# Optimization experiments

Measured on AMD Instinct MI355X. Metric: run time of the kernel, lower is better.

Reference implementation:

```python
import jax, jax.numpy as jnp
import numpy as np

B, S, C, V, LAT, NL = 256, 512, 256, 32, 256, 7
DILS = [1, 2, 4, 8, 16, 32, 64]
EPS = 1e-5


def setup_inputs() -> dict:
    key = jax.random.key(0)
    ks = jax.random.split(key, 24)
    s = 0.05
    inp = {
        "x": jax.random.randint(ks[0], (B, S), 0, V, dtype=jnp.int64 if jax.config.read("jax_enable_x64") else jnp.int32),
        "z": jax.random.normal(ks[1], (B, LAT), dtype=jnp.float32),
        "emb": jax.random.normal(ks[2], (V, C), dtype=jnp.float32) * s,
        "latent_W": jax.random.normal(ks[3], (LAT, C), dtype=jnp.float32) * s,
        "latent_b": jnp.zeros((C,), jnp.float32),
        "ln1_g": jnp.ones((NL, C), jnp.float32),
        "ln1_b": jnp.zeros((NL, C), jnp.float32),
        "w1": jax.random.normal(ks[4], (NL, C, C), jnp.float32) * s,
        "b1": jnp.zeros((NL, C), jnp.float32),
        "ln2_g": jnp.ones((NL, C), jnp.float32),
        "ln2_b": jnp.zeros((NL, C), jnp.float32),
        "wd": jax.random.normal(ks[5], (NL, 2, C, C), jnp.float32) * s,  # tap 0 = x[t-d], tap 1 = x[t]
        "bd": jnp.zeros((NL, C), jnp.float32),
        "ln3_g": jnp.ones((NL, C), jnp.float32),
        "ln3_b": jnp.zeros((NL, C), jnp.float32),
        "we": jax.random.normal(ks[6], (NL, C, C), jnp.float32) * s,
        "be": jnp.zeros((NL, C), jnp.float32),
        "wg": jax.random.normal(ks[7], (NL, C, C), jnp.float32) * s,
        "bg": jnp.zeros((NL, C), jnp.float32),
        "out_W": jax.random.normal(ks[8], (C, V), jnp.float32) * s,
        "out_b": jnp.zeros((V,), jnp.float32),
    }
    return inp


def _ln(h, g, b):
    mu = h.mean(-1, keepdims=True)
    var = jnp.mean((h - mu) ** 2, axis=-1, keepdims=True)
    return (h - mu) * jax.lax.rsqrt(var + EPS) * g + b


def _lrelu(h):
    return jnp.where(h >= 0, h, 0.01 * h)


def reference(x, z, emb, latent_W, latent_b, ln1_g, ln1_b, w1, b1,
              ln2_g, ln2_b, wd, bd, ln3_g, ln3_b, we, be, wg, bg,
              out_W, out_b):
    # channel-last layout [B, S, C] throughout (fuses away the torch transposes)
    h = emb[x] + (z @ latent_W + latent_b)[:, None, :]
    for i, d in enumerate(DILS):
        x_inp = h
        t = _lrelu(_ln(x_inp, ln1_g[i], ln1_b[i]))
        t = t @ w1[i] + b1[i]
        t = _lrelu(_ln(t, ln2_g[i], ln2_b[i]))
        # causal dilated conv, kernel=2: out[t] = W0*x[t-d] + W1*x[t]
        t_shift = jnp.pad(t, ((0, 0), (d, 0), (0, 0)))[:, :t.shape[1], :]
        t = t_shift @ wd[i, 0] + t @ wd[i, 1] + bd[i]
        t = _lrelu(_ln(t, ln3_g[i], ln3_b[i]))
        gated = (t @ we[i] + be[i]) * jax.nn.sigmoid(t @ wg[i] + bg[i])
        h = gated + x_inp
    logits = h @ out_W + out_b                      # [B, S, V]
    lp = jax.nn.log_softmax(logits, axis=-1)
    # gather log-prob of next token: lp[:, :-1, :] at x[:, 1:]
    return jnp.take_along_axis(lp[:, :-1, :], x[:, 1:, None], axis=2)[..., 0]
```

## Files before the change

### kernel.cpp

```cpp
#include <hip/hip_runtime.h>

typedef unsigned short u16;
typedef unsigned int   u32;
typedef __attribute__((ext_vector_type(8))) short short8;
typedef __attribute__((ext_vector_type(4))) float f32x4;

struct __align__(8) u16x4 { u16 x, y, z, w; };

#define NL 7
#define M_DIM 131072

__device__ __forceinline__ float b2f(u16 u) {
  union { float f; u32 i; } c; c.i = ((u32)u) << 16; return c.f;
}
__device__ __forceinline__ u16 f2b(float f) {
  union { float f; u32 i; } c; c.f = f;
  u32 r = c.i + 0x7FFFu + ((c.i >> 16) & 1u);
  return (u16)(r >> 16);
}
__device__ __forceinline__ float wave_sum(float v) {
  #pragma unroll
  for (int off = 1; off < 64; off <<= 1) v += __shfl_xor(v, off);
  return v;
}
__device__ __forceinline__ void gload16(const void* g, void* l) {
  __builtin_amdgcn_global_load_lds((const __attribute__((address_space(1))) void*)g,
                                   (__attribute__((address_space(3))) void*)l, 16, 0, 0);
}


__global__ __launch_bounds__(256) void conv_w1_k(const float* __restrict__ w1, u16* __restrict__ wT) {
  int idx = blockIdx.x * 256 + threadIdx.x;
  int i = idx >> 16, rem = idx & 65535;
  int n = rem >> 8, k = rem & 255;
  wT[idx] = f2b(w1[(i << 16) + (k << 8) + n]);
}

__global__ __launch_bounds__(256) void conv_wd_k(const float* __restrict__ wd, u16* __restrict__ wT) {
  int idx = blockIdx.x * 256 + threadIdx.x;
  int i = idx / 131072, rem = idx & 131071;
  int n = rem >> 9, k2 = rem & 511;
  int tap = k2 >> 8, k = k2 & 255;
  wT[idx] = f2b(wd[(((i * 2 + tap) << 8) + k) * 256 + n]);
}

__global__ __launch_bounds__(256) void conv_weg_k(const float* __restrict__ we, const float* __restrict__ wg,
                                                  u16* __restrict__ wT) {
  int idx = blockIdx.x * 256 + threadIdx.x;
  int i = idx / 131072, rem = idx & 131071;
  int src = rem >> 16, n = (rem >> 8) & 255, k = rem & 255;
  const float* W = src ? wg : we;
  wT[idx] = f2b(W[((i << 8) + k) * 256 + n]);
}

__global__ __launch_bounds__(256) void conv_wo_k(const float* __restrict__ outW, u16* __restrict__ wTo) {
  int idx = blockIdx.x * 256 + threadIdx.x;
  int v = idx >> 8, k = idx & 255;
  wTo[idx] = f2b(outW[k * 32 + v]);
}


__global__ __launch_bounds__(256) void zlat_k(const float* __restrict__ z, const float* __restrict__ W,
                                              const float* __restrict__ bias, float* __restrict__ zlat) {
  int b = blockIdx.x, c = threadIdx.x;
  float acc = bias[c];
  for (int l = 0; l < 256; ++l) acc += z[b * 256 + l] * W[l * 256 + c];
  zlat[b * 256 + c] = acc;
}


__device__ __forceinline__ void ln_lrelu4(float v0, float v1, float v2, float v3,
                                          const float* __restrict__ g, const float* __restrict__ b,
                                          int c, u16x4* out) {
  float s = wave_sum(v0 + v1 + v2 + v3);
  float q = wave_sum(v0 * v0 + v1 * v1 + v2 * v2 + v3 * v3);
  float mu = s * 0.00390625f;
  float var = q * 0.00390625f - mu * mu;
  float rs = rsqrtf(var + 1e-5f);
  float4 gv = *(const float4*)&g[c];
  float4 bv = *(const float4*)&b[c];
  float y0 = (v0 - mu) * rs * gv.x + bv.x; y0 = y0 >= 0.f ? y0 : 0.01f * y0;
  float y1 = (v1 - mu) * rs * gv.y + bv.y; y1 = y1 >= 0.f ? y1 : 0.01f * y1;
  float y2 = (v2 - mu) * rs * gv.z + bv.z; y2 = y2 >= 0.f ? y2 : 0.01f * y2;
  float y3 = (v3 - mu) * rs * gv.w + bv.w; y3 = y3 >= 0.f ? y3 : 0.01f * y3;
  out->x = f2b(y0); out->y = f2b(y1); out->z = f2b(y2); out->w = f2b(y3);
}


__global__ __launch_bounds__(256) void embed_ln_k(const int* __restrict__ x, const float* __restrict__ emb,
                                                  const float* __restrict__ zlat,
                                                  const float* __restrict__ g, const float* __restrict__ b,
                                                  u16* __restrict__ h, u16* __restrict__ tOut) {
  int wave = threadIdx.x >> 6, lane = threadIdx.x & 63;
  int r = blockIdx.x * 4 + wave;
  int c = lane * 4;
  int tok = x[r];
  int bi = r >> 9;
  float4 ev = *(const float4*)&emb[tok * 256 + c];
  float4 zv = *(const float4*)&zlat[bi * 256 + c];
  float v0 = ev.x + zv.x, v1 = ev.y + zv.y, v2 = ev.z + zv.z, v3 = ev.w + zv.w;
  u16x4 hb; hb.x = f2b(v0); hb.y = f2b(v1); hb.z = f2b(v2); hb.w = f2b(v3);
  *(u16x4*)&h[(long)r * 256 + c] = hb;
  u16x4 ov;
  ln_lrelu4(v0, v1, v2, v3, g, b, c, &ov);
  *(u16x4*)&tOut[(long)r * 256 + c] = ov;
}


__global__ __launch_bounds__(512, 4) void gemm_ln_k(
    const u16* __restrict__ A, const u16* __restrict__ WT, int Ktot, int dil,
    const float* __restrict__ bias, const float* __restrict__ g, const float* __restrict__ b,
    u16* __restrict__ Out)
{
  __shared__ u16 lA[128 * 32];
  __shared__ u16 lB[256 * 32];
  __shared__ float pS[128][4], pQ[128][4];
  __shared__ float muA[128], rsA[128];
  const int tid = threadIdx.x;
  const int lane = tid & 63;
  const int wv = tid >> 6;
  const int mw = wv >> 2;
  const int nw = wv & 3;
  const int m0 = blockIdx.x * 128;
  const int rA = tid >> 2;
  const int cSw = ((((tid & 3) - ((tid >> 3) & 3)) & 3)) * 8;
  const int mm = m0 + rA;
  const int s1 = mm & 511;
  const bool fixBlk = (dil > 0) && ((m0 & 511) == 0);
  const int lr = lane & 15;
  const int quad = lane >> 4;
  const int sw = ((quad + ((lr >> 1) & 3)) & 3) * 8;

  f32x4 acc[4][4];
  #pragma unroll
  for (int i = 0; i < 4; ++i)
    #pragma unroll
    for (int j = 0; j < 4; ++j) {
      acc[i][j][0] = 0.f; acc[i][j][1] = 0.f; acc[i][j][2] = 0.f; acc[i][j][3] = 0.f;
    }

  const int nkt = Ktot >> 5;
  for (int kt = 0; kt < nkt; ++kt) {
    const int kk = (kt & 7) * 32;
    int r = mm;
    if (dil > 0 && kt < 8) r = (s1 >= dil) ? (mm - dil) : mm;
    gload16(A + (long)r * 256 + kk + cSw, &lA[tid * 8]);
    const u16* bSrc = WT + kt * 32 + cSw;
    gload16(bSrc + (long)rA * Ktot,         &lB[tid * 8]);
    gload16(bSrc + (long)(rA + 128) * Ktot, &lB[tid * 8 + 4096]);
    __syncthreads();

    if (fixBlk && kt < 8) {
      if (rA < dil) {
        uint4 zz; zz.x = 0; zz.y = 0; zz.z = 0; zz.w = 0;
        *(uint4*)&lA[rA * 32 + (tid & 3) * 8] = zz;
      }
      __syncthreads();
    }

    short8 af[4], bfr[4];
    #pragma unroll
    for (int mt = 0; mt < 4; ++mt)
      af[mt] = *(const short8*)&lA[(mw * 64 + mt * 16 + lr) * 32 + sw];
    #pragma unroll
    for (int nt = 0; nt < 4; ++nt)
      bfr[nt] = *(const short8*)&lB[(nw * 64 + nt * 16 + lr) * 32 + sw];
    #pragma unroll
    for (int mt = 0; mt < 4; ++mt)
      #pragma unroll
      for (int nt = 0; nt < 4; ++nt)
        acc[mt][nt] = __builtin_amdgcn_mfma_f32_16x16x32_bf16(af[mt], bfr[nt], acc[mt][nt], 0, 0, 0);
    __syncthreads();
  }

  float biasv[4], gv[4], bv[4];
  #pragma unroll
  for (int nt = 0; nt < 4; ++nt) {
    int n = nw * 64 + nt * 16 + lr;
    biasv[nt] = bias[n]; gv[nt] = g[n]; bv[nt] = b[n];
  }
  #pragma unroll
  for (int mt = 0; mt < 4; ++mt)
    #pragma unroll
    for (int r = 0; r < 4; ++r) {
      float s = 0.f, q = 0.f;
      #pragma unroll
      for (int nt = 0; nt < 4; ++nt) {
        float v = acc[mt][nt][r] + biasv[nt];
        acc[mt][nt][r] = v;
        s += v; q += v * v;
      }
      #pragma unroll
      for (int off = 1; off < 16; off <<= 1) {
        s += __shfl_xor(s, off); q += __shfl_xor(q, off);
      }
      if (lr == 0) {
        int row = mw * 64 + mt * 16 + quad * 4 + r;
        pS[row][nw] = s; pQ[row][nw] = q;
      }
    }
  __syncthreads();
  if (tid < 128) {
    float S = pS[tid][0] + pS[tid][1] + pS[tid][2] + pS[tid][3];
    float Q = pQ[tid][0] + pQ[tid][1] + pQ[tid][2] + pQ[tid][3];
    float mu = S * 0.00390625f;
    float var = Q * 0.00390625f - mu * mu;
    muA[tid] = mu; rsA[tid] = rsqrtf(var + 1e-5f);
  }
  __syncthreads();
  #pragma unroll
  for (int mt = 0; mt < 4; ++mt)
    #pragma unroll
    for (int r = 0; r < 4; ++r) {
      int row = mw * 64 + mt * 16 + quad * 4 + r;
      float mu = muA[row], rs = rsA[row];
      #pragma unroll
      for (int nt = 0; nt < 4; ++nt) {
        float y = (acc[mt][nt][r] - mu) * rs * gv[nt] + bv[nt];
        y = y >= 0.f ? y : 0.01f * y;
        Out[(long)(m0 + row) * 256 + nw * 64 + nt * 16 + lr] = f2b(y);
      }
    }
}


__global__ __launch_bounds__(512, 4) void gemm_gate_ln_k(
    const u16* __restrict__ P, const u16* __restrict__ WTeg,
    const float* __restrict__ be, const float* __restrict__ bg,
    const float* __restrict__ g, const float* __restrict__ b,
    u16* __restrict__ h, u16* __restrict__ tOut, int doLN)
{
  __shared__ __align__(16) char smem[39424];
  u16* lA = (u16*)smem;
  u16* lB = (u16*)(smem + 4096);
  u16* xch = (u16*)smem;
  float* pS  = (float*)(smem + 36864);
  float* pQ  = (float*)(smem + 36864 + 1024);
  float* muA = (float*)(smem + 36864 + 2048);
  float* rsA = (float*)(smem + 36864 + 2304);
  const int tid = threadIdx.x;
  const int lane = tid & 63;
  const int wv = tid >> 6;
  const int eg = wv >> 2;
  const int nw = wv & 3;
  const int m0 = blockIdx.x * 64;
  const int rA = tid >> 2;
  const int cSw = ((((tid & 3) - ((tid >> 3) & 3)) & 3)) * 8;
  const int lr = lane & 15;
  const int quad = lane >> 4;
  const int sw = ((quad + ((lr >> 1) & 3)) & 3) * 8;

  f32x4 acc[4][4];
  #pragma unroll
  for (int i = 0; i < 4; ++i)
    #pragma unroll
    for (int j = 0; j < 4; ++j) {
      acc[i][j][0] = 0.f; acc[i][j][1] = 0.f; acc[i][j][2] = 0.f; acc[i][j][3] = 0.f;
    }

  for (int kt = 0; kt < 8; ++kt) {
    const int kk = kt * 32;
    if (tid < 256)
      gload16(P + (long)(m0 + rA) * 256 + kk + cSw, &lA[tid * 8]);
    const u16* bSrc = WTeg + kk + cSw;
    #pragma unroll
    for (int j = 0; j < 4; ++j)
      gload16(bSrc + (long)(rA + j * 128) * 256, &lB[tid * 8 + j * 4096]);
    __syncthreads();

    short8 af[4], bf[4];
    #pragma unroll
    for (int mt = 0; mt < 4; ++mt)
      af[mt] = *(const short8*)&lA[(mt * 16 + lr) * 32 + sw];
    #pragma unroll
    for (int nt = 0; nt < 4; ++nt)
      bf[nt] = *(const short8*)&lB[(eg * 256 + nw * 64 + nt * 16 + lr) * 32 + sw];
    #pragma unroll
    for (int mt = 0; mt < 4; ++mt)
      #pragma unroll
      for (int nt = 0; nt < 4; ++nt)
        acc[mt][nt] = __builtin_amdgcn_mfma_f32_16x16x32_bf16(af[mt], bf[nt], acc[mt][nt], 0, 0, 0);
    __syncthreads();
  }

  float bxv[4];
  #pragma unroll
  for (int nt = 0; nt < 4; ++nt) {
    int n = nw * 64 + nt * 16 + lr;
    bxv[nt] = eg ? bg[n] : be[n];
  }
  if (eg) {
    #pragma unroll
    for (int mt = 0; mt < 4; ++mt)
      #pragma unroll
      for (int r = 0; r < 4; ++r) {
        int row = mt * 16 + quad * 4 + r;
        #pragma unroll
        for (int nt = 0; nt < 4; ++nt) {
          int n = nw * 64 + nt * 16 + lr;
          float gg = acc[mt][nt][r] + bxv[nt];
          xch[row * 264 + n] = f2b(1.f / (1.f + expf(-gg)));
        }
      }
  }
  __syncthreads();
  if (!eg) {
    #pragma unroll
    for (int mt = 0; mt < 4; ++mt)
      #pragma unroll
      for (int r = 0; r < 4; ++r) {
        int row = mt * 16 + quad * 4 + r;
        long off = (long)(m0 + row) * 256;
        float s = 0.f, q = 0.f;
        #pragma unroll
        for (int nt = 0; nt < 4; ++nt) {
          int n = nw * 64 + nt * 16 + lr;
          float e = acc[mt][nt][r] + bxv[nt];
          float sg = b2f(xch[row * 264 + n]);
          float hn = e * sg + b2f(h[off + n]);
          h[off + n] = f2b(hn);
          acc[mt][nt][r] = hn;
          s += hn; q += hn * hn;
        }
        #pragma unroll
        for (int o = 1; o < 16; o <<= 1) {
          s += __shfl_xor(s, o); q += __shfl_xor(q, o);
        }
        if (lr == 0) { pS[row * 4 + nw] = s; pQ[row * 4 + nw] = q; }
      }
  }
  __syncthreads();
  if (tid < 64) {
    float S = pS[tid * 4] + pS[tid * 4 + 1] + pS[tid * 4 + 2] + pS[tid * 4 + 3];
    float Q = pQ[tid * 4] + pQ[tid * 4 + 1] + pQ[tid * 4 + 2] + pQ[tid * 4 + 3];
    float mu = S * 0.00390625f;
    float var = Q * 0.00390625f - mu * mu;
    muA[tid] = mu; rsA[tid] = rsqrtf(var + 1e-5f);
  }
  __syncthreads();
  if (doLN && !eg) {
    float gv[4], bv[4];
    #pragma unroll
    for (int nt = 0; nt < 4; ++nt) {
      int n = nw * 64 + nt * 16 + lr;
      gv[nt] = g[n]; bv[nt] = b[n];
    }
    #pragma unroll
    for (int mt = 0; mt < 4; ++mt)
      #pragma unroll
      for (int r = 0; r < 4; ++r) {
        int row = mt * 16 + quad * 4 + r;
        float mu = muA[row], rs = rsA[row];
        #pragma unroll
        for (int nt = 0; nt < 4; ++nt) {
          float y = (acc[mt][nt][r] - mu) * rs * gv[nt] + bv[nt];
          y = y >= 0.f ? y : 0.01f * y;
          tOut[(long)(m0 + row) * 256 + nw * 64 + nt * 16 + lr] = f2b(y);
        }
      }
  }
}


__global__ __launch_bounds__(256) void final_k(const u16* __restrict__ h, const u16* __restrict__ WTo,
                                               const float* __restrict__ outb, const int* __restrict__ x,
                                               float* __restrict__ out) {
  __shared__ u16 lW[32 * 264];
  const int tid = threadIdx.x;
  const int lane = tid & 63;
  const int wv = tid >> 6;
  const int mBase = blockIdx.x * 256 + wv * 64;

  #pragma unroll
  for (int j = 0; j < 4; ++j) {
    int chunk = tid + 256 * j;
    int v = chunk >> 5, k8 = chunk & 31;
    uint4 w4 = *(const uint4*)(WTo + v * 256 + k8 * 8);
    *(uint4*)&lW[v * 264 + k8 * 8] = w4;
  }
  __syncthreads();

  const int lq = (lane >> 4) * 8;
  const int lr = lane & 15;
  const int quad = lane >> 4;

  f32x4 acc[4][2];
  #pragma unroll
  for (int mt = 0; mt < 4; ++mt) {
    acc[mt][0][0] = 0.f; acc[mt][0][1] = 0.f; acc[mt][0][2] = 0.f; acc[mt][0][3] = 0.f;
    acc[mt][1][0] = 0.f; acc[mt][1][1] = 0.f; acc[mt][1][2] = 0.f; acc[mt][1][3] = 0.f;
  }

  for (int kt = 0; kt < 8; ++kt) {
    short8 bf0 = *(const short8*)&lW[lr * 264 + kt * 32 + lq];
    short8 bf1 = *(const short8*)&lW[(16 + lr) * 264 + kt * 32 + lq];
    #pragma unroll
    for (int mt = 0; mt < 4; ++mt) {
      short8 af = *(const short8*)(h + (long)(mBase + mt * 16 + lr) * 256 + kt * 32 + lq);
      acc[mt][0] = __builtin_amdgcn_mfma_f32_16x16x32_bf16(af, bf0, acc[mt][0], 0, 0, 0);
      acc[mt][1] = __builtin_amdgcn_mfma_f32_16x16x32_bf16(af, bf1, acc[mt][1], 0, 0, 0);
    }
  }

  float ob0 = outb[lr], ob1 = outb[16 + lr];
  #pragma unroll
  for (int mt = 0; mt < 4; ++mt)
    #pragma unroll
    for (int r = 0; r < 4; ++r) {
      int row = mBase + mt * 16 + quad * 4 + r;
      float lo = acc[mt][0][r] + ob0;
      float hi = acc[mt][1][r] + ob1;
      float mx = fmaxf(lo, hi);
      #pragma unroll
      for (int o = 1; o < 16; o <<= 1) mx = fmaxf(mx, __shfl_xor(mx, o));
      float se = expf(lo - mx) + expf(hi - mx);
      #pragma unroll
      for (int o = 1; o < 16; o <<= 1) se += __shfl_xor(se, o);
      int s = row & 511;
      int xa = (s == 511) ? row : (row + 1);
      int tok = x[xa];
      float lg = (tok < 16) ? lo : hi;
      float lp = lg - mx - logf(se);
      if (s != 511 && lr == (tok & 15))
        out[(row >> 9) * 511 + s] = lp;
    }
}


extern "C" void kernel_launch(void* const* d_in, const int* in_sizes, int n_in,
                              void* d_out, int out_size, void* d_ws, size_t ws_size,
                              hipStream_t stream) {
  const int*   x    = (const int*)d_in[0];
  const float* z    = (const float*)d_in[1];
  const float* emb  = (const float*)d_in[2];
  const float* latW = (const float*)d_in[3];
  const float* latb = (const float*)d_in[4];
  const float* ln1g = (const float*)d_in[5];
  const float* ln1b = (const float*)d_in[6];
  const float* w1   = (const float*)d_in[7];
  const float* b1   = (const float*)d_in[8];
  const float* ln2g = (const float*)d_in[9];
  const float* ln2b = (const float*)d_in[10];
  const float* wd   = (const float*)d_in[11];
  const float* bd   = (const float*)d_in[12];
  const float* ln3g = (const float*)d_in[13];
  const float* ln3b = (const float*)d_in[14];
  const float* we   = (const float*)d_in[15];
  const float* be   = (const float*)d_in[16];
  const float* wg   = (const float*)d_in[17];
  const float* bg   = (const float*)d_in[18];
  const float* outW = (const float*)d_in[19];
  const float* outb = (const float*)d_in[20];

  char* ws = (char*)d_ws;
  u16*   h    = (u16*)(ws + 0);
  u16*   bufA = (u16*)(ws + 67108864);
  u16*   bufB = (u16*)(ws + 134217728);
  float* zlat = (float*)(ws + 201326592);
  u16*   wT1  = (u16*)(ws + 201588736);
  u16*   wTd  = (u16*)(ws + 202506240);
  u16*   wTeg = (u16*)(ws + 204341248);
  u16*   wTo  = (u16*)(ws + 206176256);

  conv_w1_k <<<1792, 256, 0, stream>>>(w1, wT1);
  conv_wd_k <<<3584, 256, 0, stream>>>(wd, wTd);
  conv_weg_k<<<3584, 256, 0, stream>>>(we, wg, wTeg);
  conv_wo_k <<<32, 256, 0, stream>>>(outW, wTo);
  zlat_k    <<<256, 256, 0, stream>>>(z, latW, latb, zlat);
  embed_ln_k<<<M_DIM / 4, 256, 0, stream>>>(x, emb, zlat, ln1g, ln1b, h, bufA);

  u16* X = bufA;
  u16* Y = bufB;
  for (int i = 0; i < NL; ++i) {
    int d = 1 << i;
    int doLN = (i < NL - 1) ? 1 : 0;
    int ni = doLN ? (i + 1) : i;
    gemm_ln_k<<<M_DIM / 128, 512, 0, stream>>>(
        X, wT1 + i * 65536, 256, 0, b1 + i * 256, ln2g + i * 256, ln2b + i * 256, Y);
    gemm_ln_k<<<M_DIM / 128, 512, 0, stream>>>(
        Y, wTd + i * 131072, 512, d, bd + i * 256, ln3g + i * 256, ln3b + i * 256, X);
    gemm_gate_ln_k<<<M_DIM / 64, 512, 0, stream>>>(
        X, wTeg + i * 131072, be + i * 256, bg + i * 256,
        ln1g + ni * 256, ln1b + ni * 256, h, Y, doLN);
    u16* tmp = X; X = Y; Y = tmp;
  }

  final_k<<<M_DIM / 256, 256, 0, stream>>>(h, wTo, outb, x, (float*)d_out);
}
```

Baseline: 1.683 ms.

## Move LN1 into first GEMM prologue and simplify gate kernel to per-wave E/G

The LN1+LeakyReLU that used to run in the gate kernel epilogue (and in the embed kernel) now runs in a new gemm1 kernel. That kernel computes row statistics from h and normalizes A fragments on the fly while loading from global memory. The gate kernel becomes 256 threads, with each wave computing both the E and G tiles for its 64 columns. This removes the shared-memory sigmoid exchange and the LN reduction in the gate epilogue. In exchange, gemm1 reads h twice and loads its A operand unstaged from global memory. The gate kernel doubles its accumulator registers, and gemm1 runs at lower occupancy (launch bounds 512,2).

Result: slower. 1.834 ms (+8.9%).

```diff
diff --git a/kernel.cpp b/kernel.cpp
--- a/kernel.cpp
+++ b/kernel.cpp
@@ -17,11 +17,6 @@
   union { float f; u32 i; } c; c.f = f;
   u32 r = c.i + 0x7FFFu + ((c.i >> 16) & 1u);
   return (u16)(r >> 16);
-}
-__device__ __forceinline__ float wave_sum(float v) {
-  #pragma unroll
-  for (int off = 1; off < 64; off <<= 1) v += __shfl_xor(v, off);
-  return v;
 }
 __device__ __forceinline__ void gload16(const void* g, void* l) {
   __builtin_amdgcn_global_load_lds((const __attribute__((address_space(1))) void*)g,
@@ -69,28 +64,8 @@
 }
 
 
-__device__ __forceinline__ void ln_lrelu4(float v0, float v1, float v2, float v3,
-                                          const float* __restrict__ g, const float* __restrict__ b,
-                                          int c, u16x4* out) {
-  float s = wave_sum(v0 + v1 + v2 + v3);
-  float q = wave_sum(v0 * v0 + v1 * v1 + v2 * v2 + v3 * v3);
-  float mu = s * 0.00390625f;
-  float var = q * 0.00390625f - mu * mu;
-  float rs = rsqrtf(var + 1e-5f);
-  float4 gv = *(const float4*)&g[c];
-  float4 bv = *(const float4*)&b[c];
-  float y0 = (v0 - mu) * rs * gv.x + bv.x; y0 = y0 >= 0.f ? y0 : 0.01f * y0;
-  float y1 = (v1 - mu) * rs * gv.y + bv.y; y1 = y1 >= 0.f ? y1 : 0.01f * y1;
-  float y2 = (v2 - mu) * rs * gv.z + bv.z; y2 = y2 >= 0.f ? y2 : 0.01f * y2;
-  float y3 = (v3 - mu) * rs * gv.w + bv.w; y3 = y3 >= 0.f ? y3 : 0.01f * y3;
-  out->x = f2b(y0); out->y = f2b(y1); out->z = f2b(y2); out->w = f2b(y3);
-}
-
-
-__global__ __launch_bounds__(256) void embed_ln_k(const int* __restrict__ x, const float* __restrict__ emb,
-                                                  const float* __restrict__ zlat,
-                                                  const float* __restrict__ g, const float* __restrict__ b,
-                                                  u16* __restrict__ h, u16* __restrict__ tOut) {
+__global__ __launch_bounds__(256) void embed_k(const int* __restrict__ x, const float* __restrict__ emb,
+                                               const float* __restrict__ zlat, u16* __restrict__ h) {
   int wave = threadIdx.x >> 6, lane = threadIdx.x & 63;
   int r = blockIdx.x * 4 + wave;
   int c = lane * 4;
@@ -98,12 +73,162 @@
   int bi = r >> 9;
   float4 ev = *(const float4*)&emb[tok * 256 + c];
   float4 zv = *(const float4*)&zlat[bi * 256 + c];
-  float v0 = ev.x + zv.x, v1 = ev.y + zv.y, v2 = ev.z + zv.z, v3 = ev.w + zv.w;
-  u16x4 hb; hb.x = f2b(v0); hb.y = f2b(v1); hb.z = f2b(v2); hb.w = f2b(v3);
+  u16x4 hb;
+  hb.x = f2b(ev.x + zv.x); hb.y = f2b(ev.y + zv.y);
+  hb.z = f2b(ev.z + zv.z); hb.w = f2b(ev.w + zv.w);
   *(u16x4*)&h[(long)r * 256 + c] = hb;
-  u16x4 ov;
-  ln_lrelu4(v0, v1, v2, v3, g, b, c, &ov);
-  *(u16x4*)&tOut[(long)r * 256 + c] = ov;
+}
+
+
+__global__ __launch_bounds__(512, 2) void gemm1_k(
+    const u16* __restrict__ h, const u16* __restrict__ WT,
+    const float* __restrict__ lng, const float* __restrict__ lnb,
+    const float* __restrict__ bias,
+    const float* __restrict__ ln2g, const float* __restrict__ ln2b,
+    u16* __restrict__ V)
+{
+  __shared__ __align__(16) char smem[19456];
+  u16*   lB  = (u16*)smem;
+  float* muA = (float*)(smem + 16384);
+  float* rsA = (float*)(smem + 16896);
+  float* lg1 = (float*)(smem + 17408);
+  float* lb1 = (float*)(smem + 18432);
+  float* pS  = (float*)smem;
+  float* pQ  = (float*)(smem + 2048);
+  float* mu2 = (float*)(smem + 4096);
+  float* rs2 = (float*)(smem + 4608);
+
+  const int tid = threadIdx.x;
+  const int lane = tid & 63;
+  const int wv = tid >> 6;
+  const int mw = wv >> 2;
+  const int nw = wv & 3;
+  const int m0 = blockIdx.x * 128;
+  const int rA = tid >> 2;
+  const int cSw = ((((tid & 3) - ((tid >> 3) & 3)) & 3)) * 8;
+  const int lr = lane & 15;
+  const int quad = lane >> 4;
+  const int sw = ((quad + ((lr >> 1) & 3)) & 3) * 8;
+
+  if (tid < 256) { lg1[tid] = lng[tid]; lb1[tid] = lnb[tid]; }
+  {
+    const int half = lane >> 5, l5 = lane & 31;
+    #pragma unroll 2
+    for (int it = 0; it < 8; ++it) {
+      int row = wv * 16 + it * 2 + half;
+      uint4 hv = *(const uint4*)(h + (long)(m0 + row) * 256 + l5 * 8);
+      float v0 = b2f((u16)(hv.x & 0xffff)), v1 = b2f((u16)(hv.x >> 16));
+      float v2 = b2f((u16)(hv.y & 0xffff)), v3 = b2f((u16)(hv.y >> 16));
+      float v4 = b2f((u16)(hv.z & 0xffff)), v5 = b2f((u16)(hv.z >> 16));
+      float v6 = b2f((u16)(hv.w & 0xffff)), v7 = b2f((u16)(hv.w >> 16));
+      float s = v0 + v1 + v2 + v3 + v4 + v5 + v6 + v7;
+      float q = v0*v0 + v1*v1 + v2*v2 + v3*v3 + v4*v4 + v5*v5 + v6*v6 + v7*v7;
+      #pragma unroll
+      for (int o = 1; o < 32; o <<= 1) { s += __shfl_xor(s, o); q += __shfl_xor(q, o); }
+      if (l5 == 0) {
+        float mu = s * 0.00390625f;
+        float var = q * 0.00390625f - mu * mu;
+        muA[row] = mu; rsA[row] = rsqrtf(var + 1e-5f);
+      }
+    }
+  }
+  __syncthreads();
+
+  f32x4 acc[4][4];
+  #pragma unroll
+  for (int i = 0; i < 4; ++i)
+    #pragma unroll
+    for (int j = 0; j < 4; ++j) {
+      acc[i][j][0] = 0.f; acc[i][j][1] = 0.f; acc[i][j][2] = 0.f; acc[i][j][3] = 0.f;
+    }
+
+  for (int kt = 0; kt < 8; ++kt) {
+    const int kk = kt * 32;
+    const u16* bSrc = WT + kk + cSw;
+    gload16(bSrc + (long)rA * 256,         &lB[tid * 8]);
+    gload16(bSrc + (long)(rA + 128) * 256, &lB[tid * 8 + 4096]);
+    float4 g0 = *(const float4*)&lg1[kk + quad * 8];
+    float4 g1 = *(const float4*)&lg1[kk + quad * 8 + 4];
+    float4 b0 = *(const float4*)&lb1[kk + quad * 8];
+    float4 b1v = *(const float4*)&lb1[kk + quad * 8 + 4];
+    short8 af[4];
+    #pragma unroll
+    for (int mt = 0; mt < 4; ++mt) {
+      int row = mw * 64 + mt * 16 + lr;
+      short8 a = *(const short8*)(h + (long)(m0 + row) * 256 + kk + quad * 8);
+      float mu = muA[row], rs = rsA[row];
+      float y0 = (b2f((u16)a[0]) - mu) * rs * g0.x + b0.x;  y0 = y0 >= 0.f ? y0 : 0.01f * y0;
+      float y1 = (b2f((u16)a[1]) - mu) * rs * g0.y + b0.y;  y1 = y1 >= 0.f ? y1 : 0.01f * y1;
+      float y2 = (b2f((u16)a[2]) - mu) * rs * g0.z + b0.z;  y2 = y2 >= 0.f ? y2 : 0.01f * y2;
+      float y3 = (b2f((u16)a[3]) - mu) * rs * g0.w + b0.w;  y3 = y3 >= 0.f ? y3 : 0.01f * y3;
+      float y4 = (b2f((u16)a[4]) - mu) * rs * g1.x + b1v.x; y4 = y4 >= 0.f ? y4 : 0.01f * y4;
+      float y5 = (b2f((u16)a[5]) - mu) * rs * g1.y + b1v.y; y5 = y5 >= 0.f ? y5 : 0.01f * y5;
+      float y6 = (b2f((u16)a[6]) - mu) * rs * g1.z + b1v.z; y6 = y6 >= 0.f ? y6 : 0.01f * y6;
+      float y7 = (b2f((u16)a[7]) - mu) * rs * g1.w + b1v.w; y7 = y7 >= 0.f ? y7 : 0.01f * y7;
+      short8 o;
+      o[0] = (short)f2b(y0); o[1] = (short)f2b(y1); o[2] = (short)f2b(y2); o[3] = (short)f2b(y3);
+      o[4] = (short)f2b(y4); o[5] = (short)f2b(y5); o[6] = (short)f2b(y6); o[7] = (short)f2b(y7);
+      af[mt] = o;
+    }
+    __syncthreads();
+    short8 bfr[4];
+    #pragma unroll
+    for (int nt = 0; nt < 4; ++nt)
+      bfr[nt] = *(const short8*)&lB[(nw * 64 + nt * 16 + lr) * 32 + sw];
+    #pragma unroll
+    for (int mt = 0; mt < 4; ++mt)
+      #pragma unroll
+      for (int nt = 0; nt < 4; ++nt)
+        acc[mt][nt] = __builtin_amdgcn_mfma_f32_16x16x32_bf16(af[mt], bfr[nt], acc[mt][nt], 0, 0, 0);
+    __syncthreads();
+  }
+
+  float biasv[4], gv[4], bv[4];
+  #pragma unroll
+  for (int nt = 0; nt < 4; ++nt) {
+    int n = nw * 64 + nt * 16 + lr;
+    biasv[nt] = bias[n]; gv[nt] = ln2g[n]; bv[nt] = ln2b[n];
+  }
+  #pragma unroll
+  for (int mt = 0; mt < 4; ++mt)
+    #pragma unroll
+    for (int r = 0; r < 4; ++r) {
+      float s = 0.f, q = 0.f;
+      #pragma unroll
+      for (int nt = 0; nt < 4; ++nt) {
+        float v = acc[mt][nt][r] + biasv[nt];
+        acc[mt][nt][r] = v;
+        s += v; q += v * v;
+      }
+      #pragma unroll
+      for (int o = 1; o < 16; o <<= 1) { s += __shfl_xor(s, o); q += __shfl_xor(q, o); }
+      if (lr == 0) {
+        int row = mw * 64 + mt * 16 + quad * 4 + r;
+        pS[row * 4 + nw] = s; pQ[row * 4 + nw] = q;
+      }
+    }
+  __syncthreads();
+  if (tid < 128) {
+    float S = pS[tid * 4] + pS[tid * 4 + 1] + pS[tid * 4 + 2] + pS[tid * 4 + 3];
+    float Q = pQ[tid * 4] + pQ[tid * 4 + 1] + pQ[tid * 4 + 2] + pQ[tid * 4 + 3];
+    float mu = S * 0.00390625f;
+    float var = Q * 0.00390625f - mu * mu;
+    mu2[tid] = mu; rs2[tid] = rsqrtf(var + 1e-5f);
+  }
+  __syncthreads();
+  #pragma unroll
+  for (int mt = 0; mt < 4; ++mt)
+    #pragma unroll
+    for (int r = 0; r < 4; ++r) {
+      int row = mw * 64 + mt * 16 + quad * 4 + r;
+      float mu = mu2[row], rs = rs2[row];
+      #pragma unroll
+      for (int nt = 0; nt < 4; ++nt) {
+        float y = (acc[mt][nt][r] - mu) * rs * gv[nt] + bv[nt];
+        y = y >= 0.f ? y : 0.01f * y;
+        V[(long)(m0 + row) * 256 + nw * 64 + nt * 16 + lr] = f2b(y);
+      }
+    }
 }
 
 
@@ -224,25 +349,17 @@
 }
 
 
-__global__ __launch_bounds__(512, 4) void gemm_gate_ln_k(
-    const u16* __restrict__ P, const u16* __restrict__ WTeg,
-    const float* __restrict__ be, const float* __restrict__ bg,
-    const float* __restrict__ g, const float* __restrict__ b,
-    u16* __restrict__ h, u16* __restrict__ tOut, int doLN)
+__global__ __launch_bounds__(256, 2) void gate_k(
+    const u16* __restrict__ P, const u16* __restrict__ WTe, const u16* __restrict__ WTg,
+    const float* __restrict__ be, const float* __restrict__ bg, u16* __restrict__ h)
 {
-  __shared__ __align__(16) char smem[39424];
-  u16* lA = (u16*)smem;
-  u16* lB = (u16*)(smem + 4096);
-  u16* xch = (u16*)smem;
-  float* pS  = (float*)(smem + 36864);
-  float* pQ  = (float*)(smem + 36864 + 1024);
-  float* muA = (float*)(smem + 36864 + 2048);
-  float* rsA = (float*)(smem + 36864 + 2304);
+  __shared__ u16 lA[64 * 32];
+  __shared__ u16 lBe[256 * 32];
+  __shared__ u16 lBg[256 * 32];
   const int tid = threadIdx.x;
   const int lane = tid & 63;
   const int wv = tid >> 6;
-  const int eg = wv >> 2;
-  const int nw = wv & 3;
+  const int wc = wv * 64;
   const int m0 = blockIdx.x * 64;
   const int rA = tid >> 2;
   const int cSw = ((((tid & 3) - ((tid >> 3) & 3)) & 3)) * 8;
@@ -250,115 +367,66 @@
   const int quad = lane >> 4;
   const int sw = ((quad + ((lr >> 1) & 3)) & 3) * 8;
 
-  f32x4 acc[4][4];
+  f32x4 accE[4][4], accG[4][4];
   #pragma unroll
   for (int i = 0; i < 4; ++i)
     #pragma unroll
     for (int j = 0; j < 4; ++j) {
-      acc[i][j][0] = 0.f; acc[i][j][1] = 0.f; acc[i][j][2] = 0.f; acc[i][j][3] = 0.f;
+      accE[i][j][0] = 0.f; accE[i][j][1] = 0.f; accE[i][j][2] = 0.f; accE[i][j][3] = 0.f;
+      accG[i][j][0] = 0.f; accG[i][j][1] = 0.f; accG[i][j][2] = 0.f; accG[i][j][3] = 0.f;
     }
 
   for (int kt = 0; kt < 8; ++kt) {
     const int kk = kt * 32;
-    if (tid < 256)
-      gload16(P + (long)(m0 + rA) * 256 + kk + cSw, &lA[tid * 8]);
-    const u16* bSrc = WTeg + kk + cSw;
-    #pragma unroll
-    for (int j = 0; j < 4; ++j)
-      gload16(bSrc + (long)(rA + j * 128) * 256, &lB[tid * 8 + j * 4096]);
+    gload16(P + (long)(m0 + rA) * 256 + kk + cSw, &lA[tid * 8]);
+    const long bofs = (long)rA * 256 + kk + cSw;
+    #pragma unroll
+    for (int j = 0; j < 4; ++j) {
+      gload16(WTe + bofs + (long)(64 * j) * 256, &lBe[tid * 8 + j * 2048]);
+      gload16(WTg + bofs + (long)(64 * j) * 256, &lBg[tid * 8 + j * 2048]);
+    }
     __syncthreads();
 
-    short8 af[4], bf[4];
+    short8 af[4], bfe[4], bfg[4];
     #pragma unroll
     for (int mt = 0; mt < 4; ++mt)
       af[mt] = *(const short8*)&lA[(mt * 16 + lr) * 32 + sw];
     #pragma unroll
-    for (int nt = 0; nt < 4; ++nt)
-      bf[nt] = *(const short8*)&lB[(eg * 256 + nw * 64 + nt * 16 + lr) * 32 + sw];
+    for (int nt = 0; nt < 4; ++nt) {
+      bfe[nt] = *(const short8*)&lBe[(wc + nt * 16 + lr) * 32 + sw];
+      bfg[nt] = *(const short8*)&lBg[(wc + nt * 16 + lr) * 32 + sw];
+    }
     #pragma unroll
     for (int mt = 0; mt < 4; ++mt)
       #pragma unroll
-      for (int nt = 0; nt < 4; ++nt)
-        acc[mt][nt] = __builtin_amdgcn_mfma_f32_16x16x32_bf16(af[mt], bf[nt], acc[mt][nt], 0, 0, 0);
+      for (int nt = 0; nt < 4; ++nt) {
+        accE[mt][nt] = __builtin_amdgcn_mfma_f32_16x16x32_bf16(af[mt], bfe[nt], accE[mt][nt], 0, 0, 0);
+        accG[mt][nt] = __builtin_amdgcn_mfma_f32_16x16x32_bf16(af[mt], bfg[nt], accG[mt][nt], 0, 0, 0);
+      }
     __syncthreads();
   }
 
-  float bxv[4];
+  float bev[4], bgv[4];
   #pragma unroll
   for (int nt = 0; nt < 4; ++nt) {
-    int n = nw * 64 + nt * 16 + lr;
-    bxv[nt] = eg ? bg[n] : be[n];
-  }
-  if (eg) {
-    #pragma unroll
-    for (int mt = 0; mt < 4; ++mt)
-      #pragma unroll
-      for (int r = 0; r < 4; ++r) {
-        int row = mt * 16 + quad * 4 + r;
-        #pragma unroll
-        for (int nt = 0; nt < 4; ++nt) {
-          int n = nw * 64 + nt * 16 + lr;
-          float gg = acc[mt][nt][r] + bxv[nt];
-          xch[row * 264 + n] = f2b(1.f / (1.f + expf(-gg)));
-        }
-      }
-  }
-  __syncthreads();
-  if (!eg) {
-    #pragma unroll
-    for (int mt = 0; mt < 4; ++mt)
-      #pragma unroll
-      for (int r = 0; r < 4; ++r) {
-        int row = mt * 16 + quad * 4 + r;
-        long off = (long)(m0 + row) * 256;
-        float s = 0.f, q = 0.f;
-        #pragma unroll
-        for (int nt = 0; nt < 4; ++nt) {
-          int n = nw * 64 + nt * 16 + lr;
-          float e = acc[mt][nt][r] + bxv[nt];
-          float sg = b2f(xch[row * 264 + n]);
-          float hn = e * sg + b2f(h[off + n]);
-          h[off + n] = f2b(hn);
-          acc[mt][nt][r] = hn;
-          s += hn; q += hn * hn;
-        }
-        #pragma unroll
-        for (int o = 1; o < 16; o <<= 1) {
-          s += __shfl_xor(s, o); q += __shfl_xor(q, o);
-        }
-        if (lr == 0) { pS[row * 4 + nw] = s; pQ[row * 4 + nw] = q; }
-      }
-  }
-  __syncthreads();
-  if (tid < 64) {
-    float S = pS[tid * 4] + pS[tid * 4 + 1] + pS[tid * 4 + 2] + pS[tid * 4 + 3];
-    float Q = pQ[tid * 4] + pQ[tid * 4 + 1] + pQ[tid * 4 + 2] + pQ[tid * 4 + 3];
-    float mu = S * 0.00390625f;
-    float var = Q * 0.00390625f - mu * mu;
-    muA[tid] = mu; rsA[tid] = rsqrtf(var + 1e-5f);
-  }
-  __syncthreads();
-  if (doLN && !eg) {
-    float gv[4], bv[4];
-    #pragma unroll
-    for (int nt = 0; nt < 4; ++nt) {
-      int n = nw * 64 + nt * 16 + lr;
-      gv[nt] = g[n]; bv[nt] = b[n];
-    }
-    #pragma unroll
-    for (int mt = 0; mt < 4; ++mt)
-      #pragma unroll
-      for (int r = 0; r < 4; ++r) {
-        int row = mt * 16 + quad * 4 + r;
-        float mu = muA[row], rs = rsA[row];
-        #pragma unroll
-        for (int nt = 0; nt < 4; ++nt) {
-          float y = (acc[mt][nt][r] - mu) * rs * gv[nt] + bv[nt];
-          y = y >= 0.f ? y : 0.01f * y;
-          tOut[(long)(m0 + row) * 256 + nw * 64 + nt * 16 + lr] = f2b(y);
-        }
-      }
-  }
+    int n = wc + nt * 16 + lr;
+    bev[nt] = be[n]; bgv[nt] = bg[n];
+  }
+  #pragma unroll
+  for (int mt = 0; mt < 4; ++mt)
+    #pragma unroll
+    for (int r = 0; r < 4; ++r) {
+      int row = mt * 16 + quad * 4 + r;
+      long off = (long)(m0 + row) * 256;
+      #pragma unroll
+      for (int nt = 0; nt < 4; ++nt) {
+        int n = wc + nt * 16 + lr;
+        float e = accE[mt][nt][r] + bev[nt];
+        float gg = accG[mt][nt][r] + bgv[nt];
+        float hn = e * (1.f / (1.f + expf(-gg))) + b2f(h[off + n]);
+        h[off + n] = f2b(hn);
+      }
+    }
 }
 
 
@@ -467,22 +535,17 @@
   conv_weg_k<<<3584, 256, 0, stream>>>(we, wg, wTeg);
   conv_wo_k <<<32, 256, 0, stream>>>(outW, wTo);
   zlat_k    <<<256, 256, 0, stream>>>(z, latW, latb, zlat);
-  embed_ln_k<<<M_DIM / 4, 256, 0, stream>>>(x, emb, zlat, ln1g, ln1b, h, bufA);
-
-  u16* X = bufA;
-  u16* Y = bufB;
+  embed_k   <<<M_DIM / 4, 256, 0, stream>>>(x, emb, zlat, h);
+
   for (int i = 0; i < NL; ++i) {
     int d = 1 << i;
-    int doLN = (i < NL - 1) ? 1 : 0;
-    int ni = doLN ? (i + 1) : i;
+    gemm1_k<<<M_DIM / 128, 512, 0, stream>>>(
+        h, wT1 + i * 65536, ln1g + i * 256, ln1b + i * 256, b1 + i * 256,
+        ln2g + i * 256, ln2b + i * 256, bufA);
     gemm_ln_k<<<M_DIM / 128, 512, 0, stream>>>(
-        X, wT1 + i * 65536, 256, 0, b1 + i * 256, ln2g + i * 256, ln2b + i * 256, Y);
-    gemm_ln_k<<<M_DIM / 128, 512, 0, stream>>>(
-        Y, wTd + i * 131072, 512, d, bd + i * 256, ln3g + i * 256, ln3b + i * 256, X);
-    gemm_gate_ln_k<<<M_DIM / 64, 512, 0, stream>>>(
-        X, wTeg + i * 131072, be + i * 256, bg + i * 256,
-        ln1g + ni * 256, ln1b + ni * 256, h, Y, doLN);
-    u16* tmp = X; X = Y; Y = tmp;
+        bufA, wTd + i * 131072, 512, d, bd + i * 256, ln3g + i * 256, ln3b + i * 256, bufB);
+    gate_k<<<M_DIM / 64, 256, 0, stream>>>(
+        bufB, wTeg + i * 131072, wTeg + i * 131072 + 65536, be + i * 256, bg + i * 256, h);
   }
 
   final_k<<<M_DIM / 256, 256, 0, stream>>>(h, wTo, outb, x, (float*)d_out);
```
